# Performance work log

Measured on AMD Instinct MI355X. Metric: run time of the kernel, lower is better.

## Reference

```python
import jax, jax.numpy as jnp
import numpy as np

B, C_IN, N = 8, 512, 4096   # batch, input channels, timesteps
D, K = 256, 2048            # code dim (n_out), codebook size (vq_n_embed)
EMA_G = 0.99                # vq_ema_gamma


def setup_inputs() -> dict:
    key = jax.random.key(0)
    k1, k2, k3 = jax.random.split(key, 3)
    z = jax.random.normal(k1, (B, C_IN, N), jnp.float32)
    # emb: xavier_uniform with gain=10 over (K, D)
    eb = 10.0 * np.sqrt(6.0 / (K + D))
    emb = jax.random.uniform(k2, (K, D), jnp.float32, -eb, eb)
    # 1x1 Conv1d weight (no bias), xavier_uniform over (D, C_IN)
    wb = np.sqrt(6.0 / (D + C_IN))
    W = jax.random.uniform(k3, (D, C_IN), jnp.float32, -wb, wb)
    # EMA buffers as initialized in __init__
    ema_numer = emb * (1.0 - EMA_G)
    ema_denom = jnp.ones((K,), jnp.float32) * (1.0 - EMA_G)
    return {"z": z, "W": W, "emb": emb, "ema_numer": ema_numer, "ema_denom": ema_denom}


def reference(z, W, emb, ema_numer, ema_denom):
    # 1x1 conv (no bias): ze (B, D, N)
    ze = jnp.einsum('dc,bcn->bdn', W, z)
    e = jax.lax.stop_gradient(emb)  # sg(emb)
    # Squared L2 distances (B, K, N) via ||ze||^2 + ||e||^2 - 2 e.ze
    # (mathematically equal to the broadcasted (ze-e)^2 sum, without the
    #  huge (B,K,D,N) intermediate)
    ze_sq = jnp.sum(ze * ze, axis=1)              # (B, N)
    e_sq = jnp.sum(e * e, axis=1)                 # (K,)
    cross = jnp.einsum('kd,bdn->bkn', e, ze)      # (B, K, N)
    d2 = ze_sq[:, None, :] + e_sq[None, :, None] - 2.0 * cross
    min_ind = jnp.argmin(d2, axis=1)              # (B, N) int
    zq = jnp.take(e, min_ind, axis=0).transpose(0, 2, 1)  # (B, D, N)
    # ReplaceGrad straight-through: value = zq, gradient flows to ze
    out = ze + jax.lax.stop_gradient(zq - ze)
    # EMA codebook statistics (scatter-add over assignments)
    flat_ind = min_ind.reshape(-1)                          # (B*N,)
    flat_ze = ze.transpose(0, 2, 1).reshape(-1, D)          # (B*N, D)
    z_sum = jax.ops.segment_sum(flat_ze, flat_ind, num_segments=K)
    n_sum = jax.ops.segment_sum(jnp.ones((flat_ind.shape[0],), ze.dtype), flat_ind, num_segments=K)
    ema_numer_new = EMA_G * ema_numer + (1.0 - EMA_G) * z_sum
    ema_denom_new = EMA_G * ema_denom + (1.0 - EMA_G) * n_sum
    return out, ema_numer_new, ema_denom_new
```

## Files before the change

kernel.cpp:

```cpp
#include <hip/hip_runtime.h>

#define B_   8
#define CIN  512
#define NN_  4096
#define DD   256
#define KK   2048
#define KSPLIT 4
#define KPER (KK / KSPLIT)
#define NG   (B_ * NN_)

typedef _Float16 f16x8 __attribute__((ext_vector_type(8)));
typedef _Float16 f16x4 __attribute__((ext_vector_type(4)));
typedef float    f32x16 __attribute__((ext_vector_type(16)));

#define MFMA16 __builtin_amdgcn_mfma_f32_32x32x16_f16

#define GLDS16(gp, lp) __builtin_amdgcn_global_load_lds( \
    (const __attribute__((address_space(1))) void*)(gp), \
    (__attribute__((address_space(3))) void*)(lp), 16, 0, 0)

__global__ __launch_bounds__(256) void k_init(const float* __restrict__ ema_numer,
                                              float* __restrict__ out_numer,
                                              int* __restrict__ hist) {
  int i = blockIdx.x * 256 + threadIdx.x;
  if (i < KK * DD) out_numer[i] = 0.99f * ema_numer[i];
  else hist[i - KK * DD] = 0;
}

__global__ __launch_bounds__(256) void k_esq(const float* __restrict__ emb,
                                             float* __restrict__ esq,
                                             _Float16* __restrict__ emb_h,
                                             _Float16* __restrict__ emb_l) {
  int t = threadIdx.x;
  int lane = t & 63;
  int k = blockIdx.x * 4 + (t >> 6);
  float4 v = *(const float4*)&emb[(size_t)k * DD + 4 * lane];
  float s = v.x * v.x + v.y * v.y + v.z * v.z + v.w * v.w;
  f16x4 h, l;
  float* vp = (float*)&v;
#pragma unroll
  for (int i = 0; i < 4; i++) {
    _Float16 hh = (_Float16)vp[i];
    h[i] = hh;
    l[i] = (_Float16)(vp[i] - (float)hh);
  }
  *(f16x4*)&emb_h[(size_t)k * DD + 4 * lane] = h;
  *(f16x4*)&emb_l[(size_t)k * DD + 4 * lane] = l;
  for (int off = 32; off > 0; off >>= 1) s += __shfl_down(s, off, 64);
  if (lane == 0) esq[k] = s;
}

__global__ __launch_bounds__(256) void k_ze(const float* __restrict__ W,
                                            const float* __restrict__ z,
                                            _Float16* __restrict__ zeT_h,
                                            _Float16* __restrict__ zeT_l) {
  __shared__ __align__(16) char sm[69632];
  const int t = threadIdx.x;
  const int w = t >> 6, lane = t & 63;
  const int lr = lane & 31, lh = lane >> 5;
  const int wm = w & 1, wn = w >> 1;
  const int swz = (lr >> 1) & 3;
  const int b = blockIdx.z, d0 = blockIdx.y * 128, n0 = blockIdx.x * 128;

  auto stageA = [&](int buf, int c0) {
    _Float16* Ah = (_Float16*)(sm + buf * 8192);
    _Float16* Al = (_Float16*)(sm + 16384 + buf * 8192);
#pragma unroll
    for (int i = 0; i < 4; i++) {
      int fid = i * 256 + t;
      int d = fid >> 3, q8 = fid & 7;
      float4 v = *(const float4*)&W[(size_t)(d0 + d) * CIN + c0 + 4 * q8];
      float* vp = (float*)&v;
      f16x4 h, l;
#pragma unroll
      for (int e = 0; e < 4; e++) {
        _Float16 hh = (_Float16)vp[e];
        h[e] = hh;
        l[e] = (_Float16)(vp[e] - (float)hh);
      }
      int p16 = (q8 >> 1) ^ ((d >> 1) & 3);
      int off = d * 32 + p16 * 8 + (q8 & 1) * 4;
      *(f16x4*)&Ah[off] = h;
      *(f16x4*)&Al[off] = l;
    }
  };

  auto stageZ = [&](int buf, int c0) {
    const int n_l = t & 127, cg = t >> 7;
    const float* gp = z + ((size_t)b * CIN + c0 + cg * 16) * NN_ + n0 + n_l;
    float v[16];
#pragma unroll
    for (int j = 0; j < 16; j++) v[j] = gp[(size_t)j * NN_];
    _Float16* Zh = (_Float16*)(sm + 32768 + buf * 8192);
    _Float16* Zl = (_Float16*)(sm + 49152 + buf * 8192);
#pragma unroll
    for (int q = 0; q < 2; q++) {
      f16x8 h, l;
#pragma unroll
      for (int e = 0; e < 8; e++) {
        float x = v[q * 8 + e];
        _Float16 hh = (_Float16)x;
        h[e] = hh;
        l[e] = (_Float16)(x - (float)hh);
      }
      int p = (cg * 2 + q) ^ ((n_l >> 1) & 3);
      *(f16x8*)&Zh[n_l * 32 + p * 8] = h;
      *(f16x8*)&Zl[n_l * 32 + p * 8] = l;
    }
  };

  f32x16 acc[2][2];
#pragma unroll
  for (int mt = 0; mt < 2; mt++)
#pragma unroll
    for (int nt = 0; nt < 2; nt++)
#pragma unroll
      for (int i = 0; i < 16; i++) acc[mt][nt][i] = 0.0f;

  stageA(0, 0);
  stageZ(0, 0);
  int buf = 0;
  for (int c0 = 0; c0 < CIN; c0 += 32) {
    __syncthreads();
    if (c0 + 32 < CIN) { stageA(buf ^ 1, c0 + 32); stageZ(buf ^ 1, c0 + 32); }
    const _Float16* WhB = (const _Float16*)(sm + buf * 8192);
    const _Float16* WlB = (const _Float16*)(sm + 16384 + buf * 8192);
    const _Float16* ZhB = (const _Float16*)(sm + 32768 + buf * 8192);
    const _Float16* ZlB = (const _Float16*)(sm + 49152 + buf * 8192);
#pragma unroll
    for (int s = 0; s < 2; s++) {
      const int p = (2 * s + lh) ^ swz;
      const int acol = p * 8;
      const int ar0 = (wm * 64 + lr) * 32 + acol;
      const int ar1 = (wm * 64 + 32 + lr) * 32 + acol;
      const int br0 = (wn * 64 + lr) * 32 + acol;
      const int br1 = (wn * 64 + 32 + lr) * 32 + acol;
      f16x8 ah0 = *(const f16x8*)(WhB + ar0);
      f16x8 ah1 = *(const f16x8*)(WhB + ar1);
      f16x8 al0 = *(const f16x8*)(WlB + ar0);
      f16x8 al1 = *(const f16x8*)(WlB + ar1);
      f16x8 bh0 = *(const f16x8*)(ZhB + br0);
      f16x8 bh1 = *(const f16x8*)(ZhB + br1);
      f16x8 bl0 = *(const f16x8*)(ZlB + br0);
      f16x8 bl1 = *(const f16x8*)(ZlB + br1);
      acc[0][0] = MFMA16(ah0, bh0, acc[0][0], 0, 0, 0);
      acc[0][1] = MFMA16(ah0, bh1, acc[0][1], 0, 0, 0);
      acc[1][0] = MFMA16(ah1, bh0, acc[1][0], 0, 0, 0);
      acc[1][1] = MFMA16(ah1, bh1, acc[1][1], 0, 0, 0);
      acc[0][0] = MFMA16(ah0, bl0, acc[0][0], 0, 0, 0);
      acc[0][1] = MFMA16(ah0, bl1, acc[0][1], 0, 0, 0);
      acc[1][0] = MFMA16(ah1, bl0, acc[1][0], 0, 0, 0);
      acc[1][1] = MFMA16(ah1, bl1, acc[1][1], 0, 0, 0);
      acc[0][0] = MFMA16(al0, bh0, acc[0][0], 0, 0, 0);
      acc[0][1] = MFMA16(al0, bh1, acc[0][1], 0, 0, 0);
      acc[1][0] = MFMA16(al1, bh0, acc[1][0], 0, 0, 0);
      acc[1][1] = MFMA16(al1, bh1, acc[1][1], 0, 0, 0);
    }
    buf ^= 1;
  }

  __syncthreads();
  _Float16* Eh = (_Float16*)sm;
  _Float16* El = (_Float16*)(sm + 33792);
#pragma unroll
  for (int mt = 0; mt < 2; mt++)
#pragma unroll
    for (int nt = 0; nt < 2; nt++) {
      int n_l = wn * 64 + nt * 32 + lr;
#pragma unroll
      for (int g = 0; g < 4; g++) {
        int d_l = wm * 64 + mt * 32 + 8 * g + 4 * lh;
        f16x4 h, l;
#pragma unroll
        for (int e = 0; e < 4; e++) {
          float x = acc[mt][nt][4 * g + e];
          _Float16 hh = (_Float16)x;
          h[e] = hh;
          l[e] = (_Float16)(x - (float)hh);
        }
        *(f16x4*)&Eh[n_l * 132 + d_l] = h;
        *(f16x4*)&El[n_l * 132 + d_l] = l;
      }
    }
  __syncthreads();
  _Float16* gh = zeT_h + ((size_t)b * NN_ + n0) * DD + d0;
  _Float16* gl = zeT_l + ((size_t)b * NN_ + n0) * DD + d0;
#pragma unroll
  for (int i = 0; i < 16; i++) {
    int n = i * 8 + w * 2 + lh;
    int d = 4 * lr;
    *(f16x4*)&gh[(size_t)n * DD + d] = *(const f16x4*)&Eh[n * 132 + d];
    *(f16x4*)&gl[(size_t)n * DD + d] = *(const f16x4*)&El[n * 132 + d];
  }
}

__global__ __launch_bounds__(256) void k_argmin(const _Float16* __restrict__ emb_h,
                                                const _Float16* __restrict__ emb_l,
                                                const _Float16* __restrict__ zeT_h,
                                                const _Float16* __restrict__ zeT_l,
                                                const float* __restrict__ esq,
                                                float* __restrict__ pval,
                                                int* __restrict__ pidx) {
  __shared__ __align__(16) char sm[69632];
  const int t = threadIdx.x;
  const int w = t >> 6, lane = t & 63;
  const int lr = lane & 31, lh = lane >> 5;
  const int wm = w & 1, wn = w >> 1;
  const int swz = (lr >> 1) & 3;
  const int b = blockIdx.y, n0 = blockIdx.x * 128, ks = blockIdx.z;
  const int kbase = ks * KPER;

  float* esqs = (float*)(sm + 65536);
  *(float2*)&esqs[2 * t] = *(const float2*)&esq[kbase + 2 * t];

  const _Float16* zb_h = zeT_h + ((size_t)b * NN_ + n0) * DD;
  const _Float16* zb_l = zeT_l + ((size_t)b * NN_ + n0) * DD;

  auto stage = [&](int buf, int kt, int dc) {
    const int k0 = kbase + kt * 128;
    const int q = lane & 3, rr = lane >> 2;
    const int g = q ^ ((rr >> 1) & 3);
    const int rb0 = 32 * w;
#pragma unroll
    for (int j = 0; j < 2; j++) {
      int rb = rb0 + 16 * j;
      int r = rb + rr;
      int col = dc + 8 * g;
      size_t eo = (size_t)(k0 + r) * DD + col;
      size_t zo = (size_t)r * DD + col;
      char* lb = sm + (size_t)buf * 8192 + rb * 64;
      GLDS16(emb_h + eo, lb);
      GLDS16(emb_l + eo, lb + 16384);
      GLDS16(zb_h + zo, lb + 32768);
      GLDS16(zb_l + zo, lb + 49152);
    }
  };

  f32x16 vzero;
#pragma unroll
  for (int i = 0; i < 16; i++) vzero[i] = 0.0f;

  float bestv[2];
  int   besti[2];
  bestv[0] = bestv[1] = 3.4e38f;
  besti[0] = besti[1] = 0;

  stage(0, 0, 0);
  int buf = 0;
  for (int kt = 0; kt < 4; kt++) {
    f32x16 acc00 = vzero, acc01 = vzero, acc10 = vzero, acc11 = vzero;
    for (int dc = 0; dc < DD; dc += 32) {
      __syncthreads();
      if (dc + 32 < DD) stage(buf ^ 1, kt, dc + 32);
      else if (kt < 3) stage(buf ^ 1, kt + 1, 0);
      const _Float16* EHb = (const _Float16*)(sm + buf * 8192);
      const _Float16* ELb = (const _Float16*)(sm + 16384 + buf * 8192);
      const _Float16* ZHb = (const _Float16*)(sm + 32768 + buf * 8192);
      const _Float16* ZLb = (const _Float16*)(sm + 49152 + buf * 8192);
#pragma unroll
      for (int s = 0; s < 2; s++) {
        const int p = (2 * s + lh) ^ swz;
        const int acol = p * 8;
        const int ar0 = (wm * 64 + lr) * 32 + acol;
        const int ar1 = (wm * 64 + 32 + lr) * 32 + acol;
        const int br0 = (wn * 64 + lr) * 32 + acol;
        const int br1 = (wn * 64 + 32 + lr) * 32 + acol;
        f16x8 ah0 = *(const f16x8*)(EHb + ar0);
        f16x8 ah1 = *(const f16x8*)(EHb + ar1);
        f16x8 al0 = *(const f16x8*)(ELb + ar0);
        f16x8 al1 = *(const f16x8*)(ELb + ar1);
        f16x8 bh0 = *(const f16x8*)(ZHb + br0);
        f16x8 bh1 = *(const f16x8*)(ZHb + br1);
        f16x8 bl0 = *(const f16x8*)(ZLb + br0);
        f16x8 bl1 = *(const f16x8*)(ZLb + br1);
        acc00 = MFMA16(ah0, bh0, acc00, 0, 0, 0);
        acc01 = MFMA16(ah0, bh1, acc01, 0, 0, 0);
        acc10 = MFMA16(ah1, bh0, acc10, 0, 0, 0);
        acc11 = MFMA16(ah1, bh1, acc11, 0, 0, 0);
        acc00 = MFMA16(ah0, bl0, acc00, 0, 0, 0);
        acc01 = MFMA16(ah0, bl1, acc01, 0, 0, 0);
        acc10 = MFMA16(ah1, bl0, acc10, 0, 0, 0);
        acc11 = MFMA16(ah1, bl1, acc11, 0, 0, 0);
        acc00 = MFMA16(al0, bh0, acc00, 0, 0, 0);
        acc01 = MFMA16(al0, bh1, acc01, 0, 0, 0);
        acc10 = MFMA16(al1, bh0, acc10, 0, 0, 0);
        acc11 = MFMA16(al1, bh1, acc11, 0, 0, 0);
      }
      buf ^= 1;
    }
#pragma unroll
    for (int mt = 0; mt < 2; mt++)
#pragma unroll
      for (int nt = 0; nt < 2; nt++) {
        const f32x16& a = (mt == 0) ? (nt == 0 ? acc00 : acc01)
                                    : (nt == 0 ? acc10 : acc11);
#pragma unroll
        for (int r = 0; r < 16; r++) {
          int kl = kt * 128 + wm * 64 + mt * 32 + (r & 3) + 8 * (r >> 2) + 4 * lh;
          float d2 = esqs[kl] - 2.0f * a[r];
          int kg = kbase + kl;
          if (d2 < bestv[nt] || (d2 == bestv[nt] && kg < besti[nt])) {
            bestv[nt] = d2; besti[nt] = kg;
          }
        }
      }
  }

#pragma unroll
  for (int nt = 0; nt < 2; nt++) {
    float ov = __shfl_xor(bestv[nt], 32, 64);
    int   oi = __shfl_xor(besti[nt], 32, 64);
    if (ov < bestv[nt] || (ov == bestv[nt] && oi < besti[nt])) {
      bestv[nt] = ov; besti[nt] = oi;
    }
  }
  float* pv = (float*)(sm + 67584);
  int*   pi = (int*)(sm + 68608);
  __syncthreads();
  if (lh == 0) {
#pragma unroll
    for (int nt = 0; nt < 2; nt++) {
      pv[(w * 2 + nt) * 32 + lr] = bestv[nt];
      pi[(w * 2 + nt) * 32 + lr] = besti[nt];
    }
  }
  __syncthreads();
  if (t < 128) {
    int wn2 = t >> 6, nt = (t >> 5) & 1, nl = t & 31;
    int i0 = ((2 * wn2 + 0) * 2 + nt) * 32 + nl;
    int i1 = ((2 * wn2 + 1) * 2 + nt) * 32 + nl;
    float v0 = pv[i0], v1 = pv[i1];
    int   j0 = pi[i0], j1 = pi[i1];
    if (v1 < v0 || (v1 == v0 && j1 < j0)) { v0 = v1; j0 = j1; }
    size_t o = ((size_t)ks * B_ + b) * NN_ + n0 + t;
    pval[o] = v0;
    pidx[o] = j0;
  }
}

__global__ __launch_bounds__(256) void k_histm(const float* __restrict__ pval,
                                               const int* __restrict__ pidx,
                                               int* __restrict__ mind,
                                               int* __restrict__ hist) {
  __shared__ int h[KK];
  const int t = threadIdx.x;
#pragma unroll
  for (int i = 0; i < 8; i++) h[t + 256 * i] = 0;
  __syncthreads();
  const int base = blockIdx.x * 2048;
#pragma unroll
  for (int i = 0; i < 8; i++) {
    int g = base + i * 256 + t;
    float bv = pval[g];
    int   bi = pidx[g];
#pragma unroll
    for (int ks = 1; ks < KSPLIT; ks++) {
      float v = pval[(size_t)ks * NG + g];
      int  ii = pidx[(size_t)ks * NG + g];
      if (v < bv || (v == bv && ii < bi)) { bv = v; bi = ii; }
    }
    mind[g] = bi;
    atomicAdd(&h[bi], 1);
  }
  __syncthreads();
#pragma unroll
  for (int i = 0; i < 8; i++) {
    int v = h[t + 256 * i];
    if (v) atomicAdd(&hist[t + 256 * i], v);
  }
}

__global__ __launch_bounds__(256) void k_scan(const int* __restrict__ hist,
                                              const float* __restrict__ ema_denom,
                                              int* __restrict__ cursor,
                                              float* __restrict__ out_denom) {
  const float G  = 0.99f;
  const float OG = 0.009999999776482582f;
  __shared__ int ps[256];
  const int t = threadIdx.x;
  int c[8], s = 0;
#pragma unroll
  for (int e = 0; e < 8; e++) { c[e] = hist[8 * t + e]; s += c[e]; }
  ps[t] = s;
  __syncthreads();
  for (int off = 1; off < 256; off <<= 1) {
    int v = (t >= off) ? ps[t - off] : 0;
    __syncthreads();
    ps[t] += v;
    __syncthreads();
  }
  int run = ps[t] - s;
#pragma unroll
  for (int e = 0; e < 8; e++) {
    cursor[8 * t + e] = run;
    out_denom[8 * t + e] = G * ema_denom[8 * t + e] + OG * (float)c[e];
    run += c[e];
  }
}

__global__ __launch_bounds__(256) void k_out(const float* __restrict__ emb,
                                             const int* __restrict__ mind,
                                             float* __restrict__ out,
                                             int* __restrict__ cursor,
                                             int* __restrict__ sortp) {
  __shared__ __align__(16) float E[64][257];
  __shared__ int idxl[64];
  const int t = threadIdx.x;
  const int b  = blockIdx.y;
  const int n0 = blockIdx.x * 64;
  if (t < 64) idxl[t] = mind[(size_t)b * NN_ + n0 + t];
  __syncthreads();

  if (t < 64) {
    int g = b * NN_ + n0 + t;
    int k = idxl[t];
    int p = atomicAdd(&cursor[k], 1);
    sortp[p] = (k << 15) | g;
  }

  for (int i = 0; i < 16; i++) {
    int cid = t + 256 * i;
    int r = cid >> 6, q = cid & 63;
    float4 v = *(const float4*)&emb[(size_t)idxl[r] * DD + 4 * q];
    float* vp = (float*)&v;
    E[r][4 * q + 0] = vp[0];
    E[r][4 * q + 1] = vp[1];
    E[r][4 * q + 2] = vp[2];
    E[r][4 * q + 3] = vp[3];
  }
  __syncthreads();
  const int nq = t & 15, dg = t >> 4;
  float* outb = out + (size_t)b * DD * NN_ + n0;
#pragma unroll
  for (int i = 0; i < 16; i++) {
    int d = i * 16 + dg;
    float4 v = make_float4(E[4 * nq + 0][d], E[4 * nq + 1][d],
                           E[4 * nq + 2][d], E[4 * nq + 3][d]);
    *(float4*)&outb[(size_t)d * NN_ + 4 * nq] = v;
  }
}

__global__ __launch_bounds__(256) void k_zsum(const int* __restrict__ sortp,
                                              const _Float16* __restrict__ zeT_h,
                                              const _Float16* __restrict__ zeT_l,
                                              float* __restrict__ out_numer) {
  const float OG = 0.009999999776482582f;
  __shared__ int sg[256];
  const int t = threadIdx.x;
  const int w = t >> 6, lane = t & 63;
  sg[t] = sortp[blockIdx.x * 256 + t];
  __syncthreads();
  const int base = w * 64;
  float acc[4] = {0.f, 0.f, 0.f, 0.f};
  int cur = sg[base] >> 15;
  for (int j = 0; j < 64; j++) {
    int e = sg[base + j];
    int k = e >> 15, g = e & 32767;
    if (k != cur) {
      float* zs = &out_numer[(size_t)cur * DD + 4 * lane];
#pragma unroll
      for (int x = 0; x < 4; x++) { atomicAdd(&zs[x], OG * acc[x]); acc[x] = 0.f; }
      cur = k;
    }
    f16x4 h = *(const f16x4*)&zeT_h[(size_t)g * DD + 4 * lane];
    f16x4 l = *(const f16x4*)&zeT_l[(size_t)g * DD + 4 * lane];
#pragma unroll
    for (int x = 0; x < 4; x++) acc[x] += (float)h[x] + (float)l[x];
  }
  float* zs = &out_numer[(size_t)cur * DD + 4 * lane];
#pragma unroll
  for (int x = 0; x < 4; x++) atomicAdd(&zs[x], OG * acc[x]);
}

extern "C" void kernel_launch(void* const* d_in, const int* in_sizes, int n_in,
                              void* d_out, int out_size, void* d_ws, size_t ws_size,
                              hipStream_t stream) {
  (void)in_sizes; (void)n_in; (void)out_size; (void)ws_size;
  const float* z         = (const float*)d_in[0];
  const float* W         = (const float*)d_in[1];
  const float* emb       = (const float*)d_in[2];
  const float* ema_numer = (const float*)d_in[3];
  const float* ema_denom = (const float*)d_in[4];

  float* out       = (float*)d_out;
  float* out_numer = out + (size_t)B_ * DD * NN_;
  float* out_denom = out_numer + (size_t)KK * DD;

  const size_t ZET = (size_t)B_ * NN_ * DD;
  _Float16* zeT_h = (_Float16*)d_ws;
  _Float16* zeT_l = zeT_h + ZET;
  float* esq    = (float*)(zeT_l + ZET);
  int*   hist   = (int*)(esq + KK);
  int*   cursor = hist + KK;
  float* pval   = (float*)(cursor + KK);
  int*   pidx   = (int*)(pval + (size_t)KSPLIT * NG);
  int*   mind   = pidx + (size_t)KSPLIT * NG;
  int*   sortp  = mind + NG;
  _Float16* emb_h = (_Float16*)(sortp + NG);
  _Float16* emb_l = emb_h + (size_t)KK * DD;

  k_init<<<dim3((KK * DD + KK) / 256), 256, 0, stream>>>(ema_numer, out_numer, hist);
  k_esq<<<dim3(KK / 4), 256, 0, stream>>>(emb, esq, emb_h, emb_l);
  k_ze<<<dim3(NN_ / 128, DD / 128, B_), 256, 0, stream>>>(W, z, zeT_h, zeT_l);
  k_argmin<<<dim3(NN_ / 128, B_, KSPLIT), 256, 0, stream>>>(emb_h, emb_l, zeT_h, zeT_l,
                                                            esq, pval, pidx);
  k_histm<<<dim3(NG / 2048), 256, 0, stream>>>(pval, pidx, mind, hist);
  k_scan<<<dim3(1), 256, 0, stream>>>(hist, ema_denom, cursor, out_denom);
  k_out<<<dim3(NN_ / 64, B_), 256, 0, stream>>>(emb, mind, out, cursor, sortp);
  k_zsum<<<dim3(NG / 256), 256, 0, stream>>>(sortp, zeT_h, zeT_l, out_numer);
}
```

Baseline: 304.1 us.

## Pack argmin into 64-bit atomicMin and fold histogram into scan kernel

Each K-split partial argmin is packed into one 64-bit key (order-preserving float bits, then index) and reduced with atomicMin into a per-timestep slot. This removes the pval/pidx partial buffers and the separate k_histm reduction kernel. The codebook histogram now runs inside the single-block k_scan, looping over all assignments with shared-memory atomics. The two setup kernels are also merged into one launch that also initialises the atomicMin slots. This cuts launches and global traffic, but puts a serial 32K-element histogram on a single workgroup, which may be latency bound.

```diff
diff --git a/kernel.cpp b/kernel.cpp
--- a/kernel.cpp
+++ b/kernel.cpp
@@ -19,35 +19,42 @@
     (const __attribute__((address_space(1))) void*)(gp), \
     (__attribute__((address_space(3))) void*)(lp), 16, 0, 0)
 
-__global__ __launch_bounds__(256) void k_init(const float* __restrict__ ema_numer,
-                                              float* __restrict__ out_numer,
-                                              int* __restrict__ hist) {
-  int i = blockIdx.x * 256 + threadIdx.x;
-  if (i < KK * DD) out_numer[i] = 0.99f * ema_numer[i];
-  else hist[i - KK * DD] = 0;
-}
-
-__global__ __launch_bounds__(256) void k_esq(const float* __restrict__ emb,
-                                             float* __restrict__ esq,
-                                             _Float16* __restrict__ emb_h,
-                                             _Float16* __restrict__ emb_l) {
-  int t = threadIdx.x;
-  int lane = t & 63;
-  int k = blockIdx.x * 4 + (t >> 6);
-  float4 v = *(const float4*)&emb[(size_t)k * DD + 4 * lane];
-  float s = v.x * v.x + v.y * v.y + v.z * v.z + v.w * v.w;
-  f16x4 h, l;
-  float* vp = (float*)&v;
-#pragma unroll
-  for (int i = 0; i < 4; i++) {
-    _Float16 hh = (_Float16)vp[i];
-    h[i] = hh;
-    l[i] = (_Float16)(vp[i] - (float)hh);
-  }
-  *(f16x4*)&emb_h[(size_t)k * DD + 4 * lane] = h;
-  *(f16x4*)&emb_l[(size_t)k * DD + 4 * lane] = l;
-  for (int off = 32; off > 0; off >>= 1) s += __shfl_down(s, off, 64);
-  if (lane == 0) esq[k] = s;
+__device__ __forceinline__ unsigned ford(float f) {
+  unsigned u = __float_as_uint(f);
+  return (u & 0x80000000u) ? ~u : (u | 0x80000000u);
+}
+
+__global__ __launch_bounds__(256) void k_init0(const float* __restrict__ emb,
+                                               const float* __restrict__ ema_numer,
+                                               float* __restrict__ esq,
+                                               _Float16* __restrict__ emb_h,
+                                               _Float16* __restrict__ emb_l,
+                                               float* __restrict__ out_numer,
+                                               unsigned* __restrict__ mind64w) {
+  const int bid = blockIdx.x;
+  const int t = threadIdx.x;
+  if (bid < KK / 4) {
+    int lane = t & 63;
+    int k = bid * 4 + (t >> 6);
+    float4 v = *(const float4*)&emb[(size_t)k * DD + 4 * lane];
+    float s = v.x * v.x + v.y * v.y + v.z * v.z + v.w * v.w;
+    f16x4 h, l;
+    float* vp = (float*)&v;
+#pragma unroll
+    for (int i = 0; i < 4; i++) {
+      _Float16 hh = (_Float16)vp[i];
+      h[i] = hh;
+      l[i] = (_Float16)(vp[i] - (float)hh);
+    }
+    *(f16x4*)&emb_h[(size_t)k * DD + 4 * lane] = h;
+    *(f16x4*)&emb_l[(size_t)k * DD + 4 * lane] = l;
+    for (int off = 32; off > 0; off >>= 1) s += __shfl_down(s, off, 64);
+    if (lane == 0) esq[k] = s;
+  } else {
+    int i = (bid - KK / 4) * 256 + t;
+    if (i < KK * DD) out_numer[i] = 0.99f * ema_numer[i];
+    else mind64w[i - KK * DD] = 0xFFFFFFFFu;
+  }
 }
 
 __global__ __launch_bounds__(256) void k_ze(const float* __restrict__ W,
@@ -199,8 +206,7 @@
                                                 const _Float16* __restrict__ zeT_h,
                                                 const _Float16* __restrict__ zeT_l,
                                                 const float* __restrict__ esq,
-                                                float* __restrict__ pval,
-                                                int* __restrict__ pidx) {
+                                                unsigned long long* __restrict__ mind64) {
   __shared__ __align__(16) char sm[69632];
   const int t = threadIdx.x;
   const int w = t >> 6, lane = t & 63;
@@ -332,52 +338,28 @@
     float v0 = pv[i0], v1 = pv[i1];
     int   j0 = pi[i0], j1 = pi[i1];
     if (v1 < v0 || (v1 == v0 && j1 < j0)) { v0 = v1; j0 = j1; }
-    size_t o = ((size_t)ks * B_ + b) * NN_ + n0 + t;
-    pval[o] = v0;
-    pidx[o] = j0;
-  }
-}
-
-__global__ __launch_bounds__(256) void k_histm(const float* __restrict__ pval,
-                                               const int* __restrict__ pidx,
-                                               int* __restrict__ mind,
-                                               int* __restrict__ hist) {
-  __shared__ int h[KK];
-  const int t = threadIdx.x;
-#pragma unroll
-  for (int i = 0; i < 8; i++) h[t + 256 * i] = 0;
-  __syncthreads();
-  const int base = blockIdx.x * 2048;
-#pragma unroll
-  for (int i = 0; i < 8; i++) {
-    int g = base + i * 256 + t;
-    float bv = pval[g];
-    int   bi = pidx[g];
-#pragma unroll
-    for (int ks = 1; ks < KSPLIT; ks++) {
-      float v = pval[(size_t)ks * NG + g];
-      int  ii = pidx[(size_t)ks * NG + g];
-      if (v < bv || (v == bv && ii < bi)) { bv = v; bi = ii; }
-    }
-    mind[g] = bi;
-    atomicAdd(&h[bi], 1);
-  }
-  __syncthreads();
-#pragma unroll
-  for (int i = 0; i < 8; i++) {
-    int v = h[t + 256 * i];
-    if (v) atomicAdd(&hist[t + 256 * i], v);
-  }
-}
-
-__global__ __launch_bounds__(256) void k_scan(const int* __restrict__ hist,
+    unsigned long long pk = ((unsigned long long)ford(v0) << 32) | (unsigned)j0;
+    atomicMin(&mind64[(size_t)b * NN_ + n0 + t], pk);
+  }
+}
+
+__global__ __launch_bounds__(256) void k_scan(const unsigned long long* __restrict__ mind64,
                                               const float* __restrict__ ema_denom,
                                               int* __restrict__ cursor,
                                               float* __restrict__ out_denom) {
   const float G  = 0.99f;
   const float OG = 0.009999999776482582f;
+  __shared__ int hist[KK];
   __shared__ int ps[256];
   const int t = threadIdx.x;
+#pragma unroll
+  for (int i = 0; i < 8; i++) hist[t + 256 * i] = 0;
+  __syncthreads();
+  for (int i = 0; i < NG / 256; i++) {
+    int idx = (int)(mind64[i * 256 + t] & 0xFFFFFFFFULL);
+    atomicAdd(&hist[idx], 1);
+  }
+  __syncthreads();
   int c[8], s = 0;
 #pragma unroll
   for (int e = 0; e < 8; e++) { c[e] = hist[8 * t + e]; s += c[e]; }
@@ -399,7 +381,7 @@
 }
 
 __global__ __launch_bounds__(256) void k_out(const float* __restrict__ emb,
-                                             const int* __restrict__ mind,
+                                             const unsigned long long* __restrict__ mind64,
                                              float* __restrict__ out,
                                              int* __restrict__ cursor,
                                              int* __restrict__ sortp) {
@@ -408,7 +390,7 @@
   const int t = threadIdx.x;
   const int b  = blockIdx.y;
   const int n0 = blockIdx.x * 64;
-  if (t < 64) idxl[t] = mind[(size_t)b * NN_ + n0 + t];
+  if (t < 64) idxl[t] = (int)(mind64[(size_t)b * NN_ + n0 + t] & 0xFFFFFFFFULL);
   __syncthreads();
 
   if (t < 64) {
@@ -490,22 +472,19 @@
   _Float16* zeT_h = (_Float16*)d_ws;
   _Float16* zeT_l = zeT_h + ZET;
   float* esq    = (float*)(zeT_l + ZET);
-  int*   hist   = (int*)(esq + KK);
-  int*   cursor = hist + KK;
-  float* pval   = (float*)(cursor + KK);
-  int*   pidx   = (int*)(pval + (size_t)KSPLIT * NG);
-  int*   mind   = pidx + (size_t)KSPLIT * NG;
-  int*   sortp  = mind + NG;
-  _Float16* emb_h = (_Float16*)(sortp + NG);
+  int*   cursor = (int*)(esq + KK);
+  int*   sortp  = cursor + KK;
+  unsigned long long* mind64 = (unsigned long long*)(sortp + NG);
+  _Float16* emb_h = (_Float16*)(mind64 + NG);
   _Float16* emb_l = emb_h + (size_t)KK * DD;
 
-  k_init<<<dim3((KK * DD + KK) / 256), 256, 0, stream>>>(ema_numer, out_numer, hist);
-  k_esq<<<dim3(KK / 4), 256, 0, stream>>>(emb, esq, emb_h, emb_l);
+  const int initBlocks = KK / 4 + (KK * DD + 2 * NG) / 256;
+  k_init0<<<dim3(initBlocks), 256, 0, stream>>>(emb, ema_numer, esq, emb_h, emb_l,
+                                                out_numer, (unsigned*)mind64);
   k_ze<<<dim3(NN_ / 128, DD / 128, B_), 256, 0, stream>>>(W, z, zeT_h, zeT_l);
   k_argmin<<<dim3(NN_ / 128, B_, KSPLIT), 256, 0, stream>>>(emb_h, emb_l, zeT_h, zeT_l,
-                                                            esq, pval, pidx);
-  k_histm<<<dim3(NG / 2048), 256, 0, stream>>>(pval, pidx, mind, hist);
-  k_scan<<<dim3(1), 256, 0, stream>>>(hist, ema_denom, cursor, out_denom);
-  k_out<<<dim3(NN_ / 64, B_), 256, 0, stream>>>(emb, mind, out, cursor, sortp);
+                                                            esq, mind64);
+  k_scan<<<dim3(1), 256, 0, stream>>>(mind64, ema_denom, cursor, out_denom);
+  k_out<<<dim3(NN_ / 64, B_), 256, 0, stream>>>(emb, mind64, out, cursor, sortp);
   k_zsum<<<dim3(NG / 256), 256, 0, stream>>>(sortp, zeT_h, zeT_l, out_numer);
 }
```

After: 324.4 us. 6.7% more time.
